# Kernel optimization log

Hardware: AMD Instinct MI355X
Metric: run time of the kernel (lower is better)

## Reference

```python
import jax, jax.numpy as jnp
import numpy as np

N, E, B = 25000, 400000, 64
IN, HID, OUT, EDGE, TDIM, L = 16, 128, 16, 16, 64, 4
EIN = 2 * HID + 1 + EDGE  # 273


def _sinusoidal(t, dim):
    half = dim // 2
    freqs = jnp.exp(jnp.arange(half, dtype=jnp.float32) * (-np.log(10000.0) / (half - 1)))
    a = t[:, None] * freqs[None, :]
    return jnp.concatenate([jnp.sin(a), jnp.cos(a)], axis=-1)


def _layernorm(h, g, b, eps=1e-5):
    mu = h.mean(-1, keepdims=True)
    v = h.var(-1, keepdims=True)
    return (h - mu) / jnp.sqrt(v + eps) * g + b


def setup_inputs() -> dict:
    key = jax.random.key(0)
    ks = iter(jax.random.split(key, 64))

    def rn(shape, scale=0.05):
        return jax.random.normal(next(ks), shape, dtype=jnp.float32) * scale

    inp = {
        'h': jax.random.normal(next(ks), (N, IN), dtype=jnp.float32),
        'x': jax.random.normal(next(ks), (N, 3), dtype=jnp.float32),
        'edge_index': jax.random.randint(next(ks), (2, E), 0, N),
        't': jax.random.uniform(next(ks), (B,), dtype=jnp.float32) * 1000.0,
        'edge_attr': jax.random.normal(next(ks), (E, EDGE), dtype=jnp.float32),
        'batch': jnp.sort(jax.random.randint(next(ks), (N,), 0, B)),
        # embeddings
        'node_w': rn((IN, HID)), 'node_b': jnp.zeros((HID,), jnp.float32),
        'tw1': rn((TDIM, HID)), 'tb1': jnp.zeros((HID,), jnp.float32),
        'tw2': rn((HID, HID)), 'tb2': jnp.zeros((HID,), jnp.float32),
        # per-layer stacked params (L, ...)
        'edge_w1': rn((L, EIN, HID)), 'edge_b1': jnp.zeros((L, HID), jnp.float32),
        'edge_w2': rn((L, HID, HID)), 'edge_b2': jnp.zeros((L, HID), jnp.float32),
        'att_w': rn((L, HID, 1)), 'att_b': jnp.zeros((L, 1), jnp.float32),
        'cw1': rn((L, HID, HID)), 'cb1': jnp.zeros((L, HID), jnp.float32),
        'cw2': rn((L, HID, 1), scale=0.001),  # xavier gain=0.001
        'nw1': rn((L, 2 * HID, HID)), 'nb1': jnp.zeros((L, HID), jnp.float32),
        'nw2': rn((L, HID, HID)), 'nb2': jnp.zeros((L, HID), jnp.float32),
        'ln_g': jnp.ones((L, HID), jnp.float32), 'ln_b': jnp.zeros((L, HID), jnp.float32),
        # heads
        'out_w1': rn((HID, HID)), 'out_b1': jnp.zeros((HID,), jnp.float32),
        'out_w2': rn((HID, OUT)), 'out_b2': jnp.zeros((OUT,), jnp.float32),
        'head_w': rn((HID, 3), scale=0.01), 'head_b': jnp.zeros((3,), jnp.float32),
    }
    return inp


def reference(h, x, edge_index, t, edge_attr, batch,
              node_w, node_b, tw1, tb1, tw2, tb2,
              edge_w1, edge_b1, edge_w2, edge_b2, att_w, att_b,
              cw1, cb1, cw2, nw1, nb1, nw2, nb2, ln_g, ln_b,
              out_w1, out_b1, out_w2, out_b2, head_w, head_b):
    silu = jax.nn.silu
    n_nodes = h.shape[0]
    row, col = edge_index[0], edge_index[1]

    # node + time embedding
    h = h @ node_w + node_b
    te = _sinusoidal(t, TDIM)
    te = silu(te @ tw1 + tb1) @ tw2 + tb2
    h = h + te[batch]

    for i in range(L):
        coord_diff = x[row] - x[col]                      # (E, 3)
        radial = (coord_diff ** 2).sum(-1, keepdims=True)  # (E, 1)
        edge_in = jnp.concatenate([h[row], h[col], radial, edge_attr], axis=-1)
        m = silu(silu(edge_in @ edge_w1[i] + edge_b1[i]) @ edge_w2[i] + edge_b2[i])
        att = jax.nn.sigmoid(m @ att_w[i] + att_b[i])
        m = m * att
        cw = silu(m @ cw1[i] + cb1[i]) @ cw2[i]           # (E, 1)
        coord_diff = coord_diff / jnp.sqrt(radial + 1e-8)  # normalize=True
        x = x + jax.ops.segment_sum(coord_diff * cw, row, num_segments=n_nodes)
        m_i = jax.ops.segment_sum(m, row, num_segments=n_nodes)
        h_in = jnp.concatenate([h, m_i], axis=-1)
        h_new = h + (silu(h_in @ nw1[i] + nb1[i]) @ nw2[i] + nb2[i])
        h = _layernorm(h_new, ln_g[i], ln_b[i])

    h_out = silu(h @ out_w1 + out_b1) @ out_w2 + out_b2  # (N, OUT)
    x_out = h @ head_w + head_b                           # (N, 3)
    return h_out, x_out
```

## Files before the change

kernel.cpp:

```cpp
#include <hip/hip_runtime.h>
#include <cmath>

#define NN      25000
#define NEDGE   400000
#define NBATCH  64
#define IN_DIM  16
#define HID     128
#define OUT_DIM 16
#define EDGE_DIM 16
#define TDIM    64
#define NL      4
#define EIN     273
#define EPB     64
#define W1KB    36
#define W2KB    16
#define A_PAD   65
#define A3OFF   (16*A_PAD*8)

typedef short bfrag __attribute__((ext_vector_type(8)));
typedef float ffrag __attribute__((ext_vector_type(4)));

__device__ __forceinline__ float siluf(float v) { return v / (1.f + __expf(-v)); }
__device__ __forceinline__ float sigm(float v)  { return 1.f / (1.f + __expf(-v)); }
__device__ __forceinline__ unsigned short f2b(float f) {
    unsigned u = __float_as_uint(f);
    u = (u + 0x7FFFu + ((u >> 16) & 1u)) >> 16;
    return (unsigned short)u;
}
__device__ __forceinline__ float b2f(unsigned short b) {
    return __uint_as_float(((unsigned)b) << 16);
}

__global__ __launch_bounds__(256) void hist_kernel(const int* __restrict__ row, int* __restrict__ deg) {
    const int tid = blockIdx.x * 256 + threadIdx.x;
    if (tid < NEDGE) atomicAdd(&deg[row[tid]], 1);
}

__global__ __launch_bounds__(1024) void scan_kernel(const int* __restrict__ deg, int* __restrict__ row_start) {
    __shared__ int part[1024];
    const int tid = threadIdx.x;
    const int base = tid * 25;
    int sum = 0;
    for (int i = 0; i < 25; i++) { const int idx = base + i; if (idx < NN) sum += deg[idx]; }
    part[tid] = sum;
    __syncthreads();
    for (int off = 1; off < 1024; off <<= 1) {
        int v = (tid >= off) ? part[tid - off] : 0;
        __syncthreads();
        part[tid] += v;
        __syncthreads();
    }
    int run = part[tid] - sum;
    for (int i = 0; i < 25; i++) {
        const int idx = base + i;
        if (idx < NN) { row_start[idx] = run; run += deg[idx]; }
    }
    if (tid == 1023) row_start[NN] = part[1023];
}

__global__ __launch_bounds__(256) void scatter_kernel(
    const int* __restrict__ row, const int* __restrict__ col,
    const int* __restrict__ row_start, int* __restrict__ cursor,
    int* __restrict__ rowp, int* __restrict__ colp, int* __restrict__ eorder)
{
    const int tid = blockIdx.x * 256 + threadIdx.x;
    if (tid >= NEDGE) return;
    const int r = row[tid];
    const int pos = row_start[r] + atomicAdd(&cursor[r], 1);
    rowp[pos] = r; colp[pos] = col[tid]; eorder[pos] = tid;
}

__global__ __launch_bounds__(256) void ea_pack(
    const float* __restrict__ ea, const int* __restrict__ eorder, unsigned short* __restrict__ eabp)
{
    const int tid = blockIdx.x * 256 + threadIdx.x;
    if (tid >= NEDGE) return;
    const int e = eorder[tid];
    const float4* src = (const float4*)&ea[(size_t)e * 16];
    bfrag o0, o1;
    #pragma unroll
    for (int q = 0; q < 2; q++) {
        const float4 a = src[q];
        o0[q*4+0] = (short)f2b(a.x); o0[q*4+1] = (short)f2b(a.y);
        o0[q*4+2] = (short)f2b(a.z); o0[q*4+3] = (short)f2b(a.w);
    }
    #pragma unroll
    for (int q = 0; q < 2; q++) {
        const float4 a = src[2+q];
        o1[q*4+0] = (short)f2b(a.x); o1[q*4+1] = (short)f2b(a.y);
        o1[q*4+2] = (short)f2b(a.z); o1[q*4+3] = (short)f2b(a.w);
    }
    *(bfrag*)&eabp[(size_t)tid * 16]     = o0;
    *(bfrag*)&eabp[(size_t)tid * 16 + 8] = o1;
}

__global__ __launch_bounds__(256) void prep_w(
    const float* __restrict__ ew1, const float* __restrict__ ew2, const float* __restrict__ cw1,
    unsigned short* __restrict__ w1p, unsigned short* __restrict__ w2p, unsigned short* __restrict__ c1p)
{
    const int PER_L = 68 * 128;
    int tid = blockIdx.x * 256 + threadIdx.x;
    if (tid >= NL * PER_L) return;
    const int l = tid / PER_L, rem = tid % PER_L;
    const int kb = rem >> 7, n = rem & 127;
    unsigned short o[8];
    if (kb < W1KB) {
        const float* W = ew1 + (size_t)l * EIN * HID;
        #pragma unroll
        for (int j = 0; j < 8; j++) {
            const int k = kb * 8 + j;
            const int ok = (k < 256) ? k : (k < 272 ? k + 1 : (k == 272 ? 256 : -1));
            o[j] = (ok >= 0) ? f2b(W[(size_t)ok * HID + n]) : (unsigned short)0;
        }
        #pragma unroll
        for (int j = 0; j < 8; j++) w1p[(((size_t)l * W1KB + kb) * 128 + n) * 8 + j] = o[j];
    } else if (kb < W1KB + W2KB) {
        const int kb2 = kb - W1KB;
        const float* W = ew2 + (size_t)l * HID * HID;
        #pragma unroll
        for (int j = 0; j < 8; j++) o[j] = f2b(W[(size_t)(kb2 * 8 + j) * HID + n]);
        #pragma unroll
        for (int j = 0; j < 8; j++) w2p[(((size_t)l * W2KB + kb2) * 128 + n) * 8 + j] = o[j];
    } else {
        const int kb2 = kb - W1KB - W2KB;
        const float* W = cw1 + (size_t)l * HID * HID;
        #pragma unroll
        for (int j = 0; j < 8; j++) o[j] = f2b(W[(size_t)(kb2 * 8 + j) * HID + n]);
        #pragma unroll
        for (int j = 0; j < 8; j++) c1p[(((size_t)l * W2KB + kb2) * 128 + n) * 8 + j] = o[j];
    }
}

__global__ __launch_bounds__(256) void prep_w2(
    const float* __restrict__ nw1, const float* __restrict__ nw2,
    const float* __restrict__ ow1, const float* __restrict__ ow2,
    unsigned short* __restrict__ n1p, unsigned short* __restrict__ n2p,
    unsigned short* __restrict__ o1p, unsigned short* __restrict__ o2p)
{
    const int C1 = NL * 32 * 128;
    const int C2 = C1 + NL * 16 * 128;
    const int C3 = C2 + 16 * 128;
    const int C4 = C3 + 16 * 16;
    int tid = blockIdx.x * 256 + threadIdx.x;
    if (tid >= C4) return;
    if (tid < C1) {
        const int l = tid / (32*128), rem = tid % (32*128);
        const int kb = rem >> 7, n = rem & 127;
        #pragma unroll
        for (int j = 0; j < 8; j++)
            n1p[(size_t)tid*8 + j] = f2b(nw1[((size_t)l*256 + kb*8 + j)*128 + n]);
    } else if (tid < C2) {
        const int t2 = tid - C1;
        const int l = t2 / (16*128), rem = t2 % (16*128);
        const int kb = rem >> 7, n = rem & 127;
        #pragma unroll
        for (int j = 0; j < 8; j++)
            n2p[(size_t)t2*8 + j] = f2b(nw2[((size_t)l*128 + kb*8 + j)*128 + n]);
    } else if (tid < C3) {
        const int t2 = tid - C2;
        const int kb = t2 >> 7, n = t2 & 127;
        #pragma unroll
        for (int j = 0; j < 8; j++)
            o1p[(size_t)t2*8 + j] = f2b(ow1[(size_t)(kb*8 + j)*128 + n]);
    } else {
        const int t2 = tid - C3;
        const int kb = t2 >> 4, n = t2 & 15;
        #pragma unroll
        for (int j = 0; j < 8; j++)
            o2p[(size_t)t2*8 + j] = f2b(ow2[(size_t)(kb*8 + j)*16 + n]);
    }
}

__global__ __launch_bounds__(HID) void te_kernel(
    const float* __restrict__ t, const float* __restrict__ tw1, const float* __restrict__ tb1,
    const float* __restrict__ tw2, const float* __restrict__ tb2, float* __restrict__ te_out)
{
    __shared__ float s0[TDIM];
    __shared__ float s1[HID];
    const int b = blockIdx.x, j = threadIdx.x;
    const float tv = t[b];
    if (j < TDIM) {
        const int k = j & 31;
        const float freq = expf((float)k * (-logf(10000.f) / 31.f));
        const float a = tv * freq;
        s0[j] = (j < 32) ? sinf(a) : cosf(a);
    }
    __syncthreads();
    float acc = tb1[j];
    for (int k = 0; k < TDIM; k++) acc += s0[k] * tw1[k*HID + j];
    s1[j] = siluf(acc);
    __syncthreads();
    float acc2 = tb2[j];
    for (int k = 0; k < HID; k++) acc2 += s1[k] * tw2[k*HID + j];
    te_out[b*HID + j] = acc2;
}

__global__ __launch_bounds__(HID) void embed_kernel(
    const float* __restrict__ h_in, const float* __restrict__ x_in,
    const int* __restrict__ batch,
    const float* __restrict__ node_w, const float* __restrict__ node_b,
    const float* __restrict__ te, float* __restrict__ h, unsigned short* __restrict__ hbf,
    float* __restrict__ x0)
{
    __shared__ float hs[IN_DIM];
    const int n = blockIdx.x, j = threadIdx.x;
    if (j < IN_DIM) hs[j] = h_in[n*IN_DIM + j];
    if (j >= 64 && j < 67) x0[n*3 + (j - 64)] = x_in[n*3 + (j - 64)];
    __syncthreads();
    float acc = node_b[j];
    #pragma unroll
    for (int k = 0; k < IN_DIM; k++) acc += hs[k] * node_w[k*HID + j];
    acc += te[batch[n]*HID + j];
    h[n*HID + j]   = acc;
    hbf[n*HID + j] = f2b(acc);
}

__global__ __launch_bounds__(256) void edge_mfma(
    const unsigned short* __restrict__ hbf, const float* __restrict__ x,
    float* __restrict__ x_new, float* __restrict__ m_i,
    const int* __restrict__ rowp, const int* __restrict__ colp,
    const unsigned short* __restrict__ eabp,
    const unsigned short* __restrict__ W1p, const float* __restrict__ B1,
    const unsigned short* __restrict__ W2p, const float* __restrict__ B2,
    const unsigned short* __restrict__ C1p, const float* __restrict__ CB1,
    const float* __restrict__ AW, const float* __restrict__ ABv,
    const float* __restrict__ CW2)
{
    __shared__ unsigned short sA[W1KB * A_PAD * 8];
    __shared__ int rc[EPB][2];
    __shared__ float AWs[HID];
    float* scr   = (float*)sA;
    float* attS  = scr;
    float* cpart = scr + 64;

    const int t = threadIdx.x;
    const int e0 = blockIdx.x * EPB;
    const int lane = t & 63, w = t >> 6;
    const int quad = lane >> 4, colid = lane & 15;

    float cd0 = 0.f, cd1 = 0.f, cd2 = 0.f;
    if (t < EPB) {
        const int r = rowp[e0 + t], c = colp[e0 + t];
        rc[t][0] = r; rc[t][1] = c;
        const float dx = x[r*3+0] - x[c*3+0];
        const float dy = x[r*3+1] - x[c*3+1];
        const float dz = x[r*3+2] - x[c*3+2];
        const float rad = dx*dx + dy*dy + dz*dz;
        const float inv = 1.f / sqrtf(rad + 1e-8f);
        cd0 = dx*inv; cd1 = dy*inv; cd2 = dz*inv;
        unsigned short* p34 = &sA[(34*A_PAD + t) * 8];
        p34[0] = f2b(rad);
        #pragma unroll
        for (int j = 1; j < 8; j++) p34[j] = 0;
        unsigned short* p35 = &sA[(35*A_PAD + t) * 8];
        #pragma unroll
        for (int j = 0; j < 8; j++) p35[j] = 0;
    }
    if (t >= 128 && t < 256) AWs[t - 128] = AW[t - 128];
    if (t < 128) {
        const int e = t >> 1, hh = t & 1;
        *(bfrag*)&sA[((32 + hh)*A_PAD + e) * 8] = *(const bfrag*)&eabp[(size_t)(e0 + e) * 16 + hh * 8];
    }
    __syncthreads();
    #pragma unroll
    for (int it = 0; it < 8; it++) {
        const int c = t + it * 256;
        const int e = (c >> 4) & 63;
        const int half = c >> 10;
        const int kb16 = c & 15;
        const int node = rc[e][half];
        *(bfrag*)&sA[((half*16 + kb16)*A_PAD + e) * 8] = *(const bfrag*)&hbf[(size_t)node * HID + kb16 * 8];
    }
    __syncthreads();

    ffrag acc1[4][2] = {};
    for (int ks = 0; ks < 9; ks++) {
        const int kb = ks * 4 + quad;
        const bfrag b0 = *(const bfrag*)&W1p[((size_t)kb * 128 + w*32 + colid) * 8];
        const bfrag b1 = *(const bfrag*)&W1p[((size_t)kb * 128 + w*32 + 16 + colid) * 8];
        #pragma unroll
        for (int mt = 0; mt < 4; mt++) {
            const bfrag a = *(const bfrag*)&sA[(kb*A_PAD + mt*16 + colid) * 8];
            acc1[mt][0] = __builtin_amdgcn_mfma_f32_16x16x32_bf16(a, b0, acc1[mt][0], 0, 0, 0);
            acc1[mt][1] = __builtin_amdgcn_mfma_f32_16x16x32_bf16(a, b1, acc1[mt][1], 0, 0, 0);
        }
    }
    __syncthreads();
    {
        const float bias0 = B1[w*32 + colid], bias1 = B1[w*32 + 16 + colid];
        #pragma unroll
        for (int mt = 0; mt < 4; mt++)
            #pragma unroll
            for (int nt = 0; nt < 2; nt++) {
                const float bb = nt ? bias1 : bias0;
                const int f = w*32 + nt*16 + colid;
                const int kb = f >> 3, j = f & 7;
                #pragma unroll
                for (int reg = 0; reg < 4; reg++) {
                    const float v = siluf(acc1[mt][nt][reg] + bb);
                    const int e = mt*16 + quad*4 + reg;
                    sA[(kb*A_PAD + e) * 8 + j] = f2b(v);
                }
            }
    }
    __syncthreads();

    ffrag acc2[4][2] = {};
    for (int ks = 0; ks < 4; ks++) {
        const int kb = ks * 4 + quad;
        const bfrag b0 = *(const bfrag*)&W2p[((size_t)kb * 128 + w*32 + colid) * 8];
        const bfrag b1 = *(const bfrag*)&W2p[((size_t)kb * 128 + w*32 + 16 + colid) * 8];
        #pragma unroll
        for (int mt = 0; mt < 4; mt++) {
            const bfrag a = *(const bfrag*)&sA[(kb*A_PAD + mt*16 + colid) * 8];
            acc2[mt][0] = __builtin_amdgcn_mfma_f32_16x16x32_bf16(a, b0, acc2[mt][0], 0, 0, 0);
            acc2[mt][1] = __builtin_amdgcn_mfma_f32_16x16x32_bf16(a, b1, acc2[mt][1], 0, 0, 0);
        }
    }
    {
        const float bias0 = B2[w*32 + colid], bias1 = B2[w*32 + 16 + colid];
        #pragma unroll
        for (int mt = 0; mt < 4; mt++)
            #pragma unroll
            for (int nt = 0; nt < 2; nt++) {
                const float bb = nt ? bias1 : bias0;
                const int f = w*32 + nt*16 + colid;
                const int kb = f >> 3, j = f & 7;
                #pragma unroll
                for (int reg = 0; reg < 4; reg++) {
                    const float v = siluf(acc2[mt][nt][reg] + bb);
                    const int e = mt*16 + quad*4 + reg;
                    sA[A3OFF + (kb*A_PAD + e) * 8 + j] = f2b(v);
                }
            }
    }
    __syncthreads();

    {
        const int e = t >> 2, q = t & 3;
        float s = 0.f;
        #pragma unroll
        for (int kk = 0; kk < 4; kk++) {
            const int kb = q*4 + kk;
            const bfrag v = *(const bfrag*)&sA[A3OFF + (kb*A_PAD + e) * 8];
            #pragma unroll
            for (int j = 0; j < 8; j++) s += b2f((unsigned short)v[j]) * AWs[kb*8 + j];
        }
        s += __shfl_xor(s, 1);
        s += __shfl_xor(s, 2);
        if (q == 0) attS[e] = sigm(s + ABv[0]);
    }
    __syncthreads();

    ffrag acc3[4][2] = {};
    for (int ks = 0; ks < 4; ks++) {
        const int kb = ks * 4 + quad;
        const bfrag b0 = *(const bfrag*)&C1p[((size_t)kb * 128 + w*32 + colid) * 8];
        const bfrag b1 = *(const bfrag*)&C1p[((size_t)kb * 128 + w*32 + 16 + colid) * 8];
        #pragma unroll
        for (int mt = 0; mt < 4; mt++) {
            const bfrag a = *(const bfrag*)&sA[A3OFF + (kb*A_PAD + mt*16 + colid) * 8];
            acc3[mt][0] = __builtin_amdgcn_mfma_f32_16x16x32_bf16(a, b0, acc3[mt][0], 0, 0, 0);
            acc3[mt][1] = __builtin_amdgcn_mfma_f32_16x16x32_bf16(a, b1, acc3[mt][1], 0, 0, 0);
        }
    }

    {
        const int fkb0 = lane >> 3,     fj = lane & 7;
        const int fkb1 = 8 + (lane >> 3);
        float a0 = 0.f, a1 = 0.f;
        for (int i = 0; i < 16; i++) {
            const int e = (w << 4) + i;
            const float av = attS[e];
            const int r = rc[e][0];
            a0 += b2f(sA[A3OFF + (fkb0*A_PAD + e) * 8 + fj]) * av;
            a1 += b2f(sA[A3OFF + (fkb1*A_PAD + e) * 8 + fj]) * av;
            const bool flush = (i == 15) || (rc[e+1][0] != r);
            if (flush) {
                atomicAdd(&m_i[(size_t)r * HID + lane],      a0);
                atomicAdd(&m_i[(size_t)r * HID + lane + 64], a1);
                a0 = 0.f; a1 = 0.f;
            }
        }
    }

    {
        const float cb0v = CB1[w*32 + colid], cb1v = CB1[w*32 + 16 + colid];
        const float cwv0 = CW2[w*32 + colid], cwv1 = CW2[w*32 + 16 + colid];
        float att_r[4][4];
        #pragma unroll
        for (int mt = 0; mt < 4; mt++) {
            const float4 a4 = *(const float4*)&attS[mt*16 + quad*4];
            att_r[mt][0] = a4.x; att_r[mt][1] = a4.y; att_r[mt][2] = a4.z; att_r[mt][3] = a4.w;
        }
        float p[4][4];
        #pragma unroll
        for (int mt = 0; mt < 4; mt++)
            #pragma unroll
            for (int reg = 0; reg < 4; reg++) p[mt][reg] = 0.f;
        #pragma unroll
        for (int mt = 0; mt < 4; mt++)
            #pragma unroll
            for (int nt = 0; nt < 2; nt++) {
                const float cb = nt ? cb1v : cb0v;
                const float cw = nt ? cwv1 : cwv0;
                #pragma unroll
                for (int reg = 0; reg < 4; reg++)
                    p[mt][reg] += siluf(att_r[mt][reg] * acc3[mt][nt][reg] + cb) * cw;
            }
        __syncthreads();
        #pragma unroll
        for (int mt = 0; mt < 4; mt++)
            #pragma unroll
            for (int reg = 0; reg < 4; reg++) {
                float s = p[mt][reg];
                s += __shfl_xor(s, 1);
                s += __shfl_xor(s, 2);
                s += __shfl_xor(s, 4);
                s += __shfl_xor(s, 8);
                if (colid == 0) cpart[(mt*16 + quad*4 + reg) * 4 + w] = s;
            }
    }
    __syncthreads();
    if (t < EPB) {
        const float s = cpart[t*4+0] + cpart[t*4+1] + cpart[t*4+2] + cpart[t*4+3];
        const int r = rc[t][0];
        atomicAdd(&x_new[r*3+0], cd0 * s);
        atomicAdd(&x_new[r*3+1], cd1 * s);
        atomicAdd(&x_new[r*3+2], cd2 * s);
    }
}

__global__ __launch_bounds__(256) void node_mfma(
    float* __restrict__ h, unsigned short* __restrict__ hbf, const float* __restrict__ m_i,
    const unsigned short* __restrict__ N1p, const float* __restrict__ NB1,
    const unsigned short* __restrict__ N2p, const float* __restrict__ NB2,
    const float* __restrict__ LG, const float* __restrict__ LB)
{
    __shared__ unsigned short sA[32 * A_PAD * 8];
    __shared__ float mu_s[64], rs_s[64];
    float* hres = (float*)sA;

    const int t = threadIdx.x, lane = t & 63, w = t >> 6;
    const int quad = lane >> 4, colid = lane & 15;
    const int n0 = blockIdx.x * 64;

    #pragma unroll
    for (int it = 0; it < 4; it++) {
        const int c = t + it * 256;
        const int e = c >> 4, kb = c & 15;
        const int nidx = min(n0 + e, NN - 1);
        *(bfrag*)&sA[(kb*A_PAD + e) * 8] = *(const bfrag*)&hbf[(size_t)nidx * HID + kb * 8];
    }
    #pragma unroll
    for (int it = 0; it < 4; it++) {
        const int c = t + it * 256;
        const int e = c >> 4, kb = c & 15;
        const int nidx = min(n0 + e, NN - 1);
        const float4 v0 = *(const float4*)&m_i[(size_t)nidx * HID + kb * 8];
        const float4 v1 = *(const float4*)&m_i[(size_t)nidx * HID + kb * 8 + 4];
        bfrag bv;
        bv[0]=(short)f2b(v0.x); bv[1]=(short)f2b(v0.y); bv[2]=(short)f2b(v0.z); bv[3]=(short)f2b(v0.w);
        bv[4]=(short)f2b(v1.x); bv[5]=(short)f2b(v1.y); bv[6]=(short)f2b(v1.z); bv[7]=(short)f2b(v1.w);
        *(bfrag*)&sA[((16 + kb)*A_PAD + e) * 8] = bv;
    }
    __syncthreads();

    ffrag acc1[4][2] = {};
    for (int ks = 0; ks < 8; ks++) {
        const int kb = ks * 4 + quad;
        const bfrag b0 = *(const bfrag*)&N1p[((size_t)kb * 128 + w*32 + colid) * 8];
        const bfrag b1 = *(const bfrag*)&N1p[((size_t)kb * 128 + w*32 + 16 + colid) * 8];
        #pragma unroll
        for (int mt = 0; mt < 4; mt++) {
            const bfrag a = *(const bfrag*)&sA[(kb*A_PAD + mt*16 + colid) * 8];
            acc1[mt][0] = __builtin_amdgcn_mfma_f32_16x16x32_bf16(a, b0, acc1[mt][0], 0, 0, 0);
            acc1[mt][1] = __builtin_amdgcn_mfma_f32_16x16x32_bf16(a, b1, acc1[mt][1], 0, 0, 0);
        }
    }
    __syncthreads();
    {
        const float bias0 = NB1[w*32 + colid], bias1 = NB1[w*32 + 16 + colid];
        #pragma unroll
        for (int mt = 0; mt < 4; mt++)
            #pragma unroll
            for (int nt = 0; nt < 2; nt++) {
                const float bb = nt ? bias1 : bias0;
                const int f = w*32 + nt*16 + colid;
                const int kb = f >> 3, j = f & 7;
                #pragma unroll
                for (int reg = 0; reg < 4; reg++) {
                    const float v = siluf(acc1[mt][nt][reg] + bb);
                    const int e = mt*16 + quad*4 + reg;
                    sA[(kb*A_PAD + e) * 8 + j] = f2b(v);
                }
            }
    }
    __syncthreads();

    ffrag acc2[4][2] = {};
    for (int ks = 0; ks < 4; ks++) {
        const int kb = ks * 4 + quad;
        const bfrag b0 = *(const bfrag*)&N2p[((size_t)kb * 128 + w*32 + colid) * 8];
        const bfrag b1 = *(const bfrag*)&N2p[((size_t)kb * 128 + w*32 + 16 + colid) * 8];
        #pragma unroll
        for (int mt = 0; mt < 4; mt++) {
            const bfrag a = *(const bfrag*)&sA[(kb*A_PAD + mt*16 + colid) * 8];
            acc2[mt][0] = __builtin_amdgcn_mfma_f32_16x16x32_bf16(a, b0, acc2[mt][0], 0, 0, 0);
            acc2[mt][1] = __builtin_amdgcn_mfma_f32_16x16x32_bf16(a, b1, acc2[mt][1], 0, 0, 0);
        }
    }
    __syncthreads();
    {
        const float bias0 = NB2[w*32 + colid], bias1 = NB2[w*32 + 16 + colid];
        #pragma unroll
        for (int mt = 0; mt < 4; mt++)
            #pragma unroll
            for (int nt = 0; nt < 2; nt++) {
                const float bb = nt ? bias1 : bias0;
                const int f = w*32 + nt*16 + colid;
                #pragma unroll
                for (int reg = 0; reg < 4; reg++) {
                    const int row = mt*16 + quad*4 + reg;
                    const int nidx = min(n0 + row, NN - 1);
                    hres[row*129 + f] = acc2[mt][nt][reg] + bb + h[(size_t)nidx*HID + f];
                }
            }
    }
    __syncthreads();
    {
        const int row = t >> 2, q = t & 3;
        float s = 0.f, s2 = 0.f;
        #pragma unroll
        for (int i = 0; i < 32; i++) {
            const float v = hres[row*129 + q*32 + i];
            s += v; s2 += v*v;
        }
        s += __shfl_xor(s, 1); s2 += __shfl_xor(s2, 1);
        s += __shfl_xor(s, 2); s2 += __shfl_xor(s2, 2);
        if (q == 0) {
            const float mu = s * (1.f/HID);
            mu_s[row] = mu;
            rs_s[row] = rsqrtf(s2 * (1.f/HID) - mu*mu + 1e-5f);
        }
    }
    __syncthreads();
    for (int idx = t; idx < 64*HID; idx += 256) {
        const int row = idx >> 7, f = idx & 127;
        const int n = n0 + row;
        if (n < NN) {
            const float v = (hres[row*129 + f] - mu_s[row]) * rs_s[row] * LG[f] + LB[f];
            h[(size_t)n*HID + f]   = v;
            hbf[(size_t)n*HID + f] = f2b(v);
        }
    }
}

__global__ __launch_bounds__(256) void out_mfma(
    const unsigned short* __restrict__ hbf,
    const unsigned short* __restrict__ O1p, const float* __restrict__ OB1,
    const unsigned short* __restrict__ O2p, const float* __restrict__ OB2,
    const float* __restrict__ HW, const float* __restrict__ HB,
    float* __restrict__ out)
{
    __shared__ unsigned short sA[32 * A_PAD * 8];
    __shared__ float hws[HID*3];
    const int A2O = 16 * A_PAD * 8;

    const int t = threadIdx.x, lane = t & 63, w = t >> 6;
    const int quad = lane >> 4, colid = lane & 15;
    const int n0 = blockIdx.x * 64;

    if (t < 128)      { hws[t] = HW[t]; hws[t+128] = HW[t+128]; }
    else if (t < 256) { const int i = t - 128 + 256; if (i < 384) hws[i] = HW[i]; }
    #pragma unroll
    for (int it = 0; it < 4; it++) {
        const int c = t + it * 256;
        const int e = c >> 4, kb = c & 15;
        const int nidx = min(n0 + e, NN - 1);
        *(bfrag*)&sA[(kb*A_PAD + e) * 8] = *(const bfrag*)&hbf[(size_t)nidx * HID + kb * 8];
    }
    __syncthreads();

    ffrag acc1[4][2] = {};
    for (int ks = 0; ks < 4; ks++) {
        const int kb = ks * 4 + quad;
        const bfrag b0 = *(const bfrag*)&O1p[((size_t)kb * 128 + w*32 + colid) * 8];
        const bfrag b1 = *(const bfrag*)&O1p[((size_t)kb * 128 + w*32 + 16 + colid) * 8];
        #pragma unroll
        for (int mt = 0; mt < 4; mt++) {
            const bfrag a = *(const bfrag*)&sA[(kb*A_PAD + mt*16 + colid) * 8];
            acc1[mt][0] = __builtin_amdgcn_mfma_f32_16x16x32_bf16(a, b0, acc1[mt][0], 0, 0, 0);
            acc1[mt][1] = __builtin_amdgcn_mfma_f32_16x16x32_bf16(a, b1, acc1[mt][1], 0, 0, 0);
        }
    }
    {
        const float bias0 = OB1[w*32 + colid], bias1 = OB1[w*32 + 16 + colid];
        #pragma unroll
        for (int mt = 0; mt < 4; mt++)
            #pragma unroll
            for (int nt = 0; nt < 2; nt++) {
                const float bb = nt ? bias1 : bias0;
                const int f = w*32 + nt*16 + colid;
                const int kb = f >> 3, j = f & 7;
                #pragma unroll
                for (int reg = 0; reg < 4; reg++) {
                    const float v = siluf(acc1[mt][nt][reg] + bb);
                    const int e = mt*16 + quad*4 + reg;
                    sA[A2O + (kb*A_PAD + e) * 8 + j] = f2b(v);
                }
            }
    }
    __syncthreads();

    ffrag acco = {};
    for (int ks = 0; ks < 4; ks++) {
        const int kb = ks * 4 + quad;
        const bfrag a = *(const bfrag*)&sA[A2O + (kb*A_PAD + w*16 + colid) * 8];
        const bfrag b = *(const bfrag*)&O2p[((size_t)kb * 16 + colid) * 8];
        acco = __builtin_amdgcn_mfma_f32_16x16x32_bf16(a, b, acco, 0, 0, 0);
    }
    #pragma unroll
    for (int reg = 0; reg < 4; reg++) {
        const int rowg = w*16 + quad*4 + reg;
        const int n = n0 + rowg;
        if (n < NN) out[(size_t)n*OUT_DIM + colid] = acco[reg] + OB2[colid];
    }

    {
        const int rloc = t >> 2, q = t & 3;
        float s0 = 0.f, s1 = 0.f, s2 = 0.f;
        #pragma unroll
        for (int kk = 0; kk < 4; kk++) {
            const int kb = q*4 + kk;
            const bfrag v = *(const bfrag*)&sA[(kb*A_PAD + rloc) * 8];
            #pragma unroll
            for (int j = 0; j < 8; j++) {
                const float hv = b2f((unsigned short)v[j]);
                const int k = kb*8 + j;
                s0 += hv * hws[k*3+0]; s1 += hv * hws[k*3+1]; s2 += hv * hws[k*3+2];
            }
        }
        s0 += __shfl_xor(s0, 1); s1 += __shfl_xor(s1, 1); s2 += __shfl_xor(s2, 1);
        s0 += __shfl_xor(s0, 2); s1 += __shfl_xor(s1, 2); s2 += __shfl_xor(s2, 2);
        const int n = n0 + rloc;
        if (q == 0 && n < NN) {
            out[(size_t)NN*OUT_DIM + n*3 + 0] = s0 + HB[0];
            out[(size_t)NN*OUT_DIM + n*3 + 1] = s1 + HB[1];
            out[(size_t)NN*OUT_DIM + n*3 + 2] = s2 + HB[2];
        }
    }
}

extern "C" void kernel_launch(void* const* d_in, const int* in_sizes, int n_in,
                              void* d_out, int out_size, void* d_ws, size_t ws_size,
                              hipStream_t stream) {
    (void)in_sizes; (void)n_in; (void)out_size; (void)ws_size;
    const float* h_in      = (const float*)d_in[0];
    const float* x_in      = (const float*)d_in[1];
    const int*   edge_idx  = (const int*)  d_in[2];
    const float* t         = (const float*)d_in[3];
    const float* edge_attr = (const float*)d_in[4];
    const int*   batch     = (const int*)  d_in[5];
    const float* node_w = (const float*)d_in[6];
    const float* node_b = (const float*)d_in[7];
    const float* tw1    = (const float*)d_in[8];
    const float* tb1    = (const float*)d_in[9];
    const float* tw2    = (const float*)d_in[10];
    const float* tb2    = (const float*)d_in[11];
    const float* ew1    = (const float*)d_in[12];
    const float* eb1    = (const float*)d_in[13];
    const float* ew2    = (const float*)d_in[14];
    const float* eb2    = (const float*)d_in[15];
    const float* attw   = (const float*)d_in[16];
    const float* attb   = (const float*)d_in[17];
    const float* cw1    = (const float*)d_in[18];
    const float* cb1    = (const float*)d_in[19];
    const float* cw2    = (const float*)d_in[20];
    const float* nw1    = (const float*)d_in[21];
    const float* nb1    = (const float*)d_in[22];
    const float* nw2    = (const float*)d_in[23];
    const float* nb2    = (const float*)d_in[24];
    const float* lng    = (const float*)d_in[25];
    const float* lnb    = (const float*)d_in[26];
    const float* ow1    = (const float*)d_in[27];
    const float* ob1    = (const float*)d_in[28];
    const float* ow2    = (const float*)d_in[29];
    const float* ob2    = (const float*)d_in[30];
    const float* hw     = (const float*)d_in[31];
    const float* hb     = (const float*)d_in[32];

    const int* row = edge_idx;
    const int* col = edge_idx + NEDGE;

    float* ws  = (float*)d_ws;
    float* te  = ws;
    float* h   = te  + NBATCH*HID;
    float* m_i = h   + (size_t)NN*HID;
    float* x0  = m_i + (size_t)NN*HID;
    float* x1  = x0  + NN*3;
    unsigned short* hbf  = (unsigned short*)(x1 + NN*3);
    unsigned short* eabp = hbf + (size_t)NN*HID;
    unsigned short* w1p  = eabp + (size_t)NEDGE*EDGE_DIM;
    unsigned short* w2p  = w1p + (size_t)NL*W1KB*128*8;
    unsigned short* c1p  = w2p + (size_t)NL*W2KB*128*8;
    unsigned short* n1p  = c1p + (size_t)NL*W2KB*128*8;
    unsigned short* n2p  = n1p + (size_t)NL*32*128*8;
    unsigned short* o1p  = n2p + (size_t)NL*16*128*8;
    unsigned short* o2p  = o1p + (size_t)16*128*8;
    int* deg       = (int*)(o2p + 16*16*8);
    int* row_start = deg + NN;
    int* cursor    = row_start + NN + 1;
    int* rowp      = cursor + NN;
    int* colp      = rowp + NEDGE;
    int* eorder    = colp + NEDGE;

    hipMemsetAsync(deg, 0, NN*sizeof(int), stream);
    hipMemsetAsync(cursor, 0, NN*sizeof(int), stream);
    hist_kernel<<<(NEDGE+255)/256, 256, 0, stream>>>(row, deg);
    scan_kernel<<<1, 1024, 0, stream>>>(deg, row_start);
    scatter_kernel<<<(NEDGE+255)/256, 256, 0, stream>>>(row, col, row_start, cursor, rowp, colp, eorder);
    ea_pack<<<(NEDGE+255)/256, 256, 0, stream>>>(edge_attr, eorder, eabp);

    prep_w<<<(NL*68*128 + 255)/256, 256, 0, stream>>>(ew1, ew2, cw1, w1p, w2p, c1p);
    prep_w2<<<(NL*32*128 + NL*16*128 + 16*128 + 16*16 + 255)/256, 256, 0, stream>>>(
        nw1, nw2, ow1, ow2, n1p, n2p, o1p, o2p);
    te_kernel<<<NBATCH, HID, 0, stream>>>(t, tw1, tb1, tw2, tb2, te);
    embed_kernel<<<NN, HID, 0, stream>>>(h_in, x_in, batch, node_w, node_b, te, h, hbf, x0);

    const int NBLK = (NN + 63) / 64;
    float* xc = x0; float* xn = x1;
    for (int i = 0; i < NL; i++) {
        hipMemsetAsync(m_i, 0, (size_t)NN*HID*sizeof(float), stream);
        hipMemcpyAsync(xn, xc, (size_t)NN*3*sizeof(float), hipMemcpyDeviceToDevice, stream);
        edge_mfma<<<NEDGE/EPB, 256, 0, stream>>>(
            hbf, xc, xn, m_i, rowp, colp, eabp,
            w1p + (size_t)i*W1KB*128*8, eb1 + (size_t)i*HID,
            w2p + (size_t)i*W2KB*128*8, eb2 + (size_t)i*HID,
            c1p + (size_t)i*W2KB*128*8, cb1 + (size_t)i*HID,
            attw + (size_t)i*HID, attb + i,
            cw2 + (size_t)i*HID);
        node_mfma<<<NBLK, 256, 0, stream>>>(
            h, hbf, m_i,
            n1p + (size_t)i*32*128*8, nb1 + (size_t)i*HID,
            n2p + (size_t)i*16*128*8, nb2 + (size_t)i*HID,
            lng + (size_t)i*HID,      lnb + (size_t)i*HID);
        float* tmp = xc; xc = xn; xn = tmp;
    }

    out_mfma<<<NBLK, 256, 0, stream>>>(hbf, o1p, ob1, o2p, ob2, hw, hb, (float*)d_out);
}
```

Before: 1.198 ms.

## Interleave weight columns for paired bf16 stores and halve node tile size

Output columns of the edge and node MLP weights are permuted during packing, so each lane's two MFMA output tiles hold adjacent features. The epilogues can then write bf16x2 pairs to shared memory and read float2 residuals. The node kernel also moves from 64 to 32 nodes per block, which doubles the block count for better occupancy and load spread, at the cost of reloading weights more often. The LayerNorm reduction is reworked to use 8 threads per row.

```diff
diff --git a/kernel.cpp b/kernel.cpp
--- a/kernel.cpp
+++ b/kernel.cpp
@@ -1,4 +1,5 @@
 #include <hip/hip_runtime.h>
+#include <hip/hip_bf16.h>
 #include <cmath>
 
 #define NN      25000
@@ -16,6 +17,8 @@
 #define W2KB    16
 #define A_PAD   65
 #define A3OFF   (16*A_PAD*8)
+#define NPB     32
+#define NPAD    33
 
 typedef short bfrag __attribute__((ext_vector_type(8)));
 typedef float ffrag __attribute__((ext_vector_type(4)));
@@ -29,6 +32,9 @@
 }
 __device__ __forceinline__ float b2f(unsigned short b) {
     return __uint_as_float(((unsigned)b) << 16);
+}
+__device__ __forceinline__ int ileave(int n) {
+    return (n & 0x60) | ((n & 15) << 1) | ((n >> 4) & 1);
 }
 
 __global__ __launch_bounds__(256) void hist_kernel(const int* __restrict__ row, int* __restrict__ deg) {
@@ -106,19 +112,21 @@
     unsigned short o[8];
     if (kb < W1KB) {
         const float* W = ew1 + (size_t)l * EIN * HID;
+        const int nc = ileave(n);
         #pragma unroll
         for (int j = 0; j < 8; j++) {
             const int k = kb * 8 + j;
             const int ok = (k < 256) ? k : (k < 272 ? k + 1 : (k == 272 ? 256 : -1));
-            o[j] = (ok >= 0) ? f2b(W[(size_t)ok * HID + n]) : (unsigned short)0;
+            o[j] = (ok >= 0) ? f2b(W[(size_t)ok * HID + nc]) : (unsigned short)0;
         }
         #pragma unroll
         for (int j = 0; j < 8; j++) w1p[(((size_t)l * W1KB + kb) * 128 + n) * 8 + j] = o[j];
     } else if (kb < W1KB + W2KB) {
         const int kb2 = kb - W1KB;
         const float* W = ew2 + (size_t)l * HID * HID;
-        #pragma unroll
-        for (int j = 0; j < 8; j++) o[j] = f2b(W[(size_t)(kb2 * 8 + j) * HID + n]);
+        const int nc = ileave(n);
+        #pragma unroll
+        for (int j = 0; j < 8; j++) o[j] = f2b(W[(size_t)(kb2 * 8 + j) * HID + nc]);
         #pragma unroll
         for (int j = 0; j < 8; j++) w2p[(((size_t)l * W2KB + kb2) * 128 + n) * 8 + j] = o[j];
     } else {
@@ -146,16 +154,18 @@
     if (tid < C1) {
         const int l = tid / (32*128), rem = tid % (32*128);
         const int kb = rem >> 7, n = rem & 127;
+        const int nc = ileave(n);
         #pragma unroll
         for (int j = 0; j < 8; j++)
-            n1p[(size_t)tid*8 + j] = f2b(nw1[((size_t)l*256 + kb*8 + j)*128 + n]);
+            n1p[(size_t)tid*8 + j] = f2b(nw1[((size_t)l*256 + kb*8 + j)*128 + nc]);
     } else if (tid < C2) {
         const int t2 = tid - C1;
         const int l = t2 / (16*128), rem = t2 % (16*128);
         const int kb = rem >> 7, n = rem & 127;
+        const int nc = ileave(n);
         #pragma unroll
         for (int j = 0; j < 8; j++)
-            n2p[(size_t)t2*8 + j] = f2b(nw2[((size_t)l*128 + kb*8 + j)*128 + n]);
+            n2p[(size_t)t2*8 + j] = f2b(nw2[((size_t)l*128 + kb*8 + j)*128 + nc]);
     } else if (tid < C3) {
         const int t2 = tid - C2;
         const int kb = t2 >> 7, n = t2 & 127;
@@ -287,20 +297,18 @@
     }
     __syncthreads();
     {
-        const float bias0 = B1[w*32 + colid], bias1 = B1[w*32 + 16 + colid];
+        const int f0 = w*32 + 2*colid;
+        const int kb = f0 >> 3, j = f0 & 7;
+        const float b0v = B1[f0], b1v = B1[f0+1];
         #pragma unroll
         for (int mt = 0; mt < 4; mt++)
             #pragma unroll
-            for (int nt = 0; nt < 2; nt++) {
-                const float bb = nt ? bias1 : bias0;
-                const int f = w*32 + nt*16 + colid;
-                const int kb = f >> 3, j = f & 7;
-                #pragma unroll
-                for (int reg = 0; reg < 4; reg++) {
-                    const float v = siluf(acc1[mt][nt][reg] + bb);
-                    const int e = mt*16 + quad*4 + reg;
-                    sA[(kb*A_PAD + e) * 8 + j] = f2b(v);
-                }
+            for (int reg = 0; reg < 4; reg++) {
+                const float v0 = siluf(acc1[mt][0][reg] + b0v);
+                const float v1 = siluf(acc1[mt][1][reg] + b1v);
+                const int e = mt*16 + quad*4 + reg;
+                *(__hip_bfloat162*)&sA[(kb*A_PAD + e) * 8 + j] =
+                    __float22bfloat162_rn(make_float2(v0, v1));
             }
     }
     __syncthreads();
@@ -318,20 +326,18 @@
         }
     }
     {
-        const float bias0 = B2[w*32 + colid], bias1 = B2[w*32 + 16 + colid];
+        const int f0 = w*32 + 2*colid;
+        const int kb = f0 >> 3, j = f0 & 7;
+        const float b0v = B2[f0], b1v = B2[f0+1];
         #pragma unroll
         for (int mt = 0; mt < 4; mt++)
             #pragma unroll
-            for (int nt = 0; nt < 2; nt++) {
-                const float bb = nt ? bias1 : bias0;
-                const int f = w*32 + nt*16 + colid;
-                const int kb = f >> 3, j = f & 7;
-                #pragma unroll
-                for (int reg = 0; reg < 4; reg++) {
-                    const float v = siluf(acc2[mt][nt][reg] + bb);
-                    const int e = mt*16 + quad*4 + reg;
-                    sA[A3OFF + (kb*A_PAD + e) * 8 + j] = f2b(v);
-                }
+            for (int reg = 0; reg < 4; reg++) {
+                const float v0 = siluf(acc2[mt][0][reg] + b0v);
+                const float v1 = siluf(acc2[mt][1][reg] + b1v);
+                const int e = mt*16 + quad*4 + reg;
+                *(__hip_bfloat162*)&sA[A3OFF + (kb*A_PAD + e) * 8 + j] =
+                    __float22bfloat162_rn(make_float2(v0, v1));
             }
     }
     __syncthreads();
@@ -437,23 +443,23 @@
     const unsigned short* __restrict__ N2p, const float* __restrict__ NB2,
     const float* __restrict__ LG, const float* __restrict__ LB)
 {
-    __shared__ unsigned short sA[32 * A_PAD * 8];
-    __shared__ float mu_s[64], rs_s[64];
+    __shared__ unsigned short sA[32 * NPAD * 8];
+    __shared__ float mu_s[NPB], rs_s[NPB];
     float* hres = (float*)sA;
 
     const int t = threadIdx.x, lane = t & 63, w = t >> 6;
     const int quad = lane >> 4, colid = lane & 15;
-    const int n0 = blockIdx.x * 64;
+    const int n0 = blockIdx.x * NPB;
 
     #pragma unroll
-    for (int it = 0; it < 4; it++) {
+    for (int it = 0; it < 2; it++) {
         const int c = t + it * 256;
         const int e = c >> 4, kb = c & 15;
         const int nidx = min(n0 + e, NN - 1);
-        *(bfrag*)&sA[(kb*A_PAD + e) * 8] = *(const bfrag*)&hbf[(size_t)nidx * HID + kb * 8];
+        *(bfrag*)&sA[(kb*NPAD + e) * 8] = *(const bfrag*)&hbf[(size_t)nidx * HID + kb * 8];
     }
     #pragma unroll
-    for (int it = 0; it < 4; it++) {
+    for (int it = 0; it < 2; it++) {
         const int c = t + it * 256;
         const int e = c >> 4, kb = c & 15;
         const int nidx = min(n0 + e, NN - 1);
@@ -462,82 +468,81 @@
         bfrag bv;
         bv[0]=(short)f2b(v0.x); bv[1]=(short)f2b(v0.y); bv[2]=(short)f2b(v0.z); bv[3]=(short)f2b(v0.w);
         bv[4]=(short)f2b(v1.x); bv[5]=(short)f2b(v1.y); bv[6]=(short)f2b(v1.z); bv[7]=(short)f2b(v1.w);
-        *(bfrag*)&sA[((16 + kb)*A_PAD + e) * 8] = bv;
-    }
-    __syncthreads();
-
-    ffrag acc1[4][2] = {};
+        *(bfrag*)&sA[((16 + kb)*NPAD + e) * 8] = bv;
+    }
+    __syncthreads();
+
+    ffrag acc1[2][2] = {};
     for (int ks = 0; ks < 8; ks++) {
         const int kb = ks * 4 + quad;
         const bfrag b0 = *(const bfrag*)&N1p[((size_t)kb * 128 + w*32 + colid) * 8];
         const bfrag b1 = *(const bfrag*)&N1p[((size_t)kb * 128 + w*32 + 16 + colid) * 8];
         #pragma unroll
-        for (int mt = 0; mt < 4; mt++) {
-            const bfrag a = *(const bfrag*)&sA[(kb*A_PAD + mt*16 + colid) * 8];
+        for (int mt = 0; mt < 2; mt++) {
+            const bfrag a = *(const bfrag*)&sA[(kb*NPAD + mt*16 + colid) * 8];
             acc1[mt][0] = __builtin_amdgcn_mfma_f32_16x16x32_bf16(a, b0, acc1[mt][0], 0, 0, 0);
             acc1[mt][1] = __builtin_amdgcn_mfma_f32_16x16x32_bf16(a, b1, acc1[mt][1], 0, 0, 0);
         }
     }
     __syncthreads();
     {
-        const float bias0 = NB1[w*32 + colid], bias1 = NB1[w*32 + 16 + colid];
-        #pragma unroll
-        for (int mt = 0; mt < 4; mt++)
-            #pragma unroll
-            for (int nt = 0; nt < 2; nt++) {
-                const float bb = nt ? bias1 : bias0;
-                const int f = w*32 + nt*16 + colid;
-                const int kb = f >> 3, j = f & 7;
-                #pragma unroll
-                for (int reg = 0; reg < 4; reg++) {
-                    const float v = siluf(acc1[mt][nt][reg] + bb);
-                    const int e = mt*16 + quad*4 + reg;
-                    sA[(kb*A_PAD + e) * 8 + j] = f2b(v);
-                }
-            }
-    }
-    __syncthreads();
-
-    ffrag acc2[4][2] = {};
+        const int f0 = w*32 + 2*colid;
+        const int kb = f0 >> 3, j = f0 & 7;
+        const float b0v = NB1[f0], b1v = NB1[f0+1];
+        #pragma unroll
+        for (int mt = 0; mt < 2; mt++)
+            #pragma unroll
+            for (int reg = 0; reg < 4; reg++) {
+                const float v0 = siluf(acc1[mt][0][reg] + b0v);
+                const float v1 = siluf(acc1[mt][1][reg] + b1v);
+                const int e = mt*16 + quad*4 + reg;
+                *(__hip_bfloat162*)&sA[(kb*NPAD + e) * 8 + j] =
+                    __float22bfloat162_rn(make_float2(v0, v1));
+            }
+    }
+    __syncthreads();
+
+    ffrag acc2[2][2] = {};
     for (int ks = 0; ks < 4; ks++) {
         const int kb = ks * 4 + quad;
         const bfrag b0 = *(const bfrag*)&N2p[((size_t)kb * 128 + w*32 + colid) * 8];
         const bfrag b1 = *(const bfrag*)&N2p[((size_t)kb * 128 + w*32 + 16 + colid) * 8];
         #pragma unroll
-        for (int mt = 0; mt < 4; mt++) {
-            const bfrag a = *(const bfrag*)&sA[(kb*A_PAD + mt*16 + colid) * 8];
+        for (int mt = 0; mt < 2; mt++) {
+            const bfrag a = *(const bfrag*)&sA[(kb*NPAD + mt*16 + colid) * 8];
             acc2[mt][0] = __builtin_amdgcn_mfma_f32_16x16x32_bf16(a, b0, acc2[mt][0], 0, 0, 0);
             acc2[mt][1] = __builtin_amdgcn_mfma_f32_16x16x32_bf16(a, b1, acc2[mt][1], 0, 0, 0);
         }
     }
     __syncthreads();
     {
-        const float bias0 = NB2[w*32 + colid], bias1 = NB2[w*32 + 16 + colid];
-        #pragma unroll
-        for (int mt = 0; mt < 4; mt++)
-            #pragma unroll
-            for (int nt = 0; nt < 2; nt++) {
-                const float bb = nt ? bias1 : bias0;
-                const int f = w*32 + nt*16 + colid;
-                #pragma unroll
-                for (int reg = 0; reg < 4; reg++) {
-                    const int row = mt*16 + quad*4 + reg;
-                    const int nidx = min(n0 + row, NN - 1);
-                    hres[row*129 + f] = acc2[mt][nt][reg] + bb + h[(size_t)nidx*HID + f];
-                }
-            }
-    }
-    __syncthreads();
-    {
-        const int row = t >> 2, q = t & 3;
+        const int f0 = w*32 + 2*colid;
+        const float b0v = NB2[f0], b1v = NB2[f0+1];
+        #pragma unroll
+        for (int mt = 0; mt < 2; mt++)
+            #pragma unroll
+            for (int reg = 0; reg < 4; reg++) {
+                const int row = mt*16 + quad*4 + reg;
+                const int nidx = min(n0 + row, NN - 1);
+                const float2 hr = *(const float2*)&h[(size_t)nidx*HID + f0];
+                float2 o;
+                o.x = acc2[mt][0][reg] + b0v + hr.x;
+                o.y = acc2[mt][1][reg] + b1v + hr.y;
+                *(float2*)&hres[row*130 + f0] = o;
+            }
+    }
+    __syncthreads();
+    {
+        const int row = t >> 3, q = t & 7;
         float s = 0.f, s2 = 0.f;
         #pragma unroll
-        for (int i = 0; i < 32; i++) {
-            const float v = hres[row*129 + q*32 + i];
+        for (int i = 0; i < 16; i++) {
+            const float v = hres[row*130 + q*16 + i];
             s += v; s2 += v*v;
         }
         s += __shfl_xor(s, 1); s2 += __shfl_xor(s2, 1);
         s += __shfl_xor(s, 2); s2 += __shfl_xor(s2, 2);
+        s += __shfl_xor(s, 4); s2 += __shfl_xor(s2, 4);
         if (q == 0) {
             const float mu = s * (1.f/HID);
             mu_s[row] = mu;
@@ -545,11 +550,11 @@
         }
     }
     __syncthreads();
-    for (int idx = t; idx < 64*HID; idx += 256) {
+    for (int idx = t; idx < NPB*HID; idx += 256) {
         const int row = idx >> 7, f = idx & 127;
         const int n = n0 + row;
         if (n < NN) {
-            const float v = (hres[row*129 + f] - mu_s[row]) * rs_s[row] * LG[f] + LB[f];
+            const float v = (hres[row*130 + f] - mu_s[row]) * rs_s[row] * LG[f] + LB[f];
             h[(size_t)n*HID + f]   = v;
             hbf[(size_t)n*HID + f] = f2b(v);
         }
@@ -728,7 +733,8 @@
     te_kernel<<<NBATCH, HID, 0, stream>>>(t, tw1, tb1, tw2, tb2, te);
     embed_kernel<<<NN, HID, 0, stream>>>(h_in, x_in, batch, node_w, node_b, te, h, hbf, x0);
 
-    const int NBLK = (NN + 63) / 64;
+    const int NBLK = (NN + NPB - 1) / NPB;
+    const int OBLK = (NN + 63) / 64;
     float* xc = x0; float* xn = x1;
     for (int i = 0; i < NL; i++) {
         hipMemsetAsync(m_i, 0, (size_t)NN*HID*sizeof(float), stream);
@@ -748,5 +754,5 @@
         float* tmp = xc; xc = xn; xn = tmp;
     }
 
-    out_mfma<<<NBLK, 256, 0, stream>>>(hbf, o1p, ob1, o2p, ob2, hw, hb, (float*)d_out);
-}
+    out_mfma<<<OBLK, 256, 0, stream>>>(hbf, o1p, ob1, o2p, ob2, hw, hb, (float*)d_out);
+}
```

After: 1.083 ms. 1.11x faster.
